# Performance work log

Hardware: AMD Instinct MI355X
Metric: run time of the kernel (lower is better)

The kernel has to match this reference:

```python
import jax, jax.numpy as jnp
import numpy as np

B, CQ, CKV, H, W = 16, 512, 512, 48, 48
NH = 8
HD = CQ // NH
SCALE = HD ** -0.5


def setup_inputs() -> dict:
    key = jax.random.key(0)
    ks = jax.random.split(key, 11)
    s = 0.02
    return {
        "query_features": jax.random.normal(ks[0], (B, CQ, H, W), jnp.float32),
        "key_features": jax.random.normal(ks[1], (B, CKV, H, W), jnp.float32),
        "value_features": jax.random.normal(ks[2], (B, CKV, H, W), jnp.float32),
        "Wq": jax.random.normal(ks[3], (CQ, CQ), jnp.float32) * s,
        "bq": jnp.zeros((CQ,), jnp.float32),
        "Wk": jax.random.normal(ks[4], (CQ, CKV), jnp.float32) * s,
        "bk": jnp.zeros((CQ,), jnp.float32),
        "Wv": jax.random.normal(ks[5], (CQ, CKV), jnp.float32) * s,
        "bv": jnp.zeros((CQ,), jnp.float32),
        "Wo": jax.random.normal(ks[6], (CQ, CQ), jnp.float32) * s,
        "bo": jnp.zeros((CQ,), jnp.float32),
    }


def _proj(x, Wt, b):
    # 1x1 conv == channel GEMM: (O,C) x (B,C,H,W) -> (B,O,H,W)
    return jnp.einsum('oc,bchw->bohw', Wt, x) + b[None, :, None, None]


def reference(query_features, key_features, value_features,
              Wq, bq, Wk, bk, Wv, bv, Wo, bo):
    b, cq, h, w = query_features.shape
    hw = h * w
    Q = _proj(query_features, Wq, bq).reshape(b, NH, HD, hw)
    K = _proj(key_features, Wk, bk).reshape(b, NH, HD, hw)
    V = _proj(value_features, Wv, bv).reshape(b, NH, HD, hw)
    # NOTE: faithful to source — contraction is over the SPATIAL axis d=H*W,
    # so scores are (B, NH, HD, HD) (head_dim x head_dim attention).
    scores = jnp.einsum('bnhd,bnkd->bnhk', Q, K) * SCALE
    attn = jax.nn.softmax(scores, axis=-1)
    out = jnp.einsum('bnhk,bnkd->bnhd', attn, V)  # (B, NH, HD, HW)
    out = out.reshape(b, cq, h, w)
    return _proj(out, Wo, bo)
```

## Files before the change

### kernel.cpp

```cpp
#include <hip/hip_runtime.h>
#include <hip/hip_bf16.h>

#define B_   16
#define C_   512
#define HW_  2304
#define NH_  8
#define SCALE_ 0.125f

typedef __bf16 bf16x8 __attribute__((ext_vector_type(8)));
typedef __bf16 bf16x4 __attribute__((ext_vector_type(4)));
typedef float  f32x4  __attribute__((ext_vector_type(4)));

#define MFMA16(a, b, c) __builtin_amdgcn_mfma_f32_16x16x32_bf16((a), (b), (c), 0, 0, 0)

__device__ __forceinline__ void gload_lds16(const void* g, void* l) {
    __builtin_amdgcn_global_load_lds(
        (const __attribute__((address_space(1))) unsigned int*)g,
        (__attribute__((address_space(3))) unsigned int*)l, 16, 0, 0);
}

__device__ __forceinline__ bf16x8 pack8(const float4 a, const float4 b) {
    bf16x8 o;
    o[0] = (__bf16)a.x; o[1] = (__bf16)a.y; o[2] = (__bf16)a.z; o[3] = (__bf16)a.w;
    o[4] = (__bf16)b.x; o[5] = (__bf16)b.y; o[6] = (__bf16)b.z; o[7] = (__bf16)b.w;
    return o;
}

__global__ __launch_bounds__(256) void wprep(
    const float* __restrict__ Wq, const float* __restrict__ Wk,
    const float* __restrict__ Wv, const float* __restrict__ Wo,
    __bf16* __restrict__ WqB, __bf16* __restrict__ WkB,
    __bf16* __restrict__ WvT, __bf16* __restrict__ WoB)
{
    const int t = threadIdx.x;
    if (blockIdx.y < 3) {
        const float* src = blockIdx.y == 0 ? Wq : blockIdx.y == 1 ? Wk : Wo;
        __bf16*      dst = blockIdx.y == 0 ? WqB : blockIdx.y == 1 ? WkB : WoB;
        const int idx = blockIdx.x * 2048 + t * 8;
        const float4 f0 = *(const float4*)&src[idx];
        const float4 f1 = *(const float4*)&src[idx + 4];
        *(bf16x8*)&dst[idx] = pack8(f0, f1);
        return;
    }
    if (blockIdx.x >= 64) return;
    const int tx = blockIdx.x & 7, ty = blockIdx.x >> 3;
    __shared__ float Ts[64 * 65];
    {
        const int r = t >> 2, c0 = (t & 3) * 16;
        #pragma unroll
        for (int j = 0; j < 4; ++j) {
            const float4 v = *(const float4*)&Wv[(size_t)(ty * 64 + r) * C_ + tx * 64 + c0 + j * 4];
            Ts[r * 65 + c0 + j * 4 + 0] = v.x;
            Ts[r * 65 + c0 + j * 4 + 1] = v.y;
            Ts[r * 65 + c0 + j * 4 + 2] = v.z;
            Ts[r * 65 + c0 + j * 4 + 3] = v.w;
        }
    }
    __syncthreads();
    {
        const int c = t >> 2, r0 = (t & 3) * 16;
        bf16x8 o0, o1;
        #pragma unroll
        for (int j = 0; j < 8; ++j) {
            o0[j] = (__bf16)Ts[(r0 + j) * 65 + c];
            o1[j] = (__bf16)Ts[(r0 + 8 + j) * 65 + c];
        }
        *(bf16x8*)&WvT[(size_t)(tx * 64 + c) * C_ + ty * 64 + r0]     = o0;
        *(bf16x8*)&WvT[(size_t)(tx * 64 + c) * C_ + ty * 64 + r0 + 8] = o1;
    }
}

__global__ __launch_bounds__(256) void prep(
    const float* __restrict__ X, __bf16* __restrict__ XT)
{
    const int t  = threadIdx.x;
    const int b  = blockIdx.z;
    const int c0 = blockIdx.y * 64;
    const int h0 = blockIdx.x * 128;
    const float* Xb = X + (size_t)b * C_ * HW_;
    __bf16* XTb = XT + (size_t)b * HW_ * C_;

    __shared__ float Ts[64 * 129];

    #pragma unroll
    for (int p = 0; p < 8; ++p) {
        const int c  = p * 8 + (t >> 5);
        const int hg = (t & 31) * 4;
        const float4 v = *(const float4*)&Xb[(size_t)(c0 + c) * HW_ + h0 + hg];
        Ts[c * 129 + hg + 0] = v.x;
        Ts[c * 129 + hg + 1] = v.y;
        Ts[c * 129 + hg + 2] = v.z;
        Ts[c * 129 + hg + 3] = v.w;
    }
    __syncthreads();
    #pragma unroll
    for (int p = 0; p < 4; ++p) {
        const int hw = p * 32 + (t >> 3);
        const int g  = (t & 7) * 8;
        bf16x8 o;
        #pragma unroll
        for (int e = 0; e < 8; ++e)
            o[e] = (__bf16)Ts[(g + e) * 129 + hw];
        *(bf16x8*)&XTb[(size_t)(h0 + hw) * C_ + c0 + g] = o;
    }
}

__global__ __launch_bounds__(512) void gxx(
    const float* __restrict__ Xk, const float* __restrict__ Xq,
    __bf16* __restrict__ Gp, float* __restrict__ xksum, float* __restrict__ xqsum)
{
    const int i    = blockIdx.x;
    const int xcd  = i & 7, slot = i >> 3;
    const int b    = xcd + 8 * (slot & 1);
    const int xy   = slot >> 1;
    const int n0   = (xy & 3) * 128;
    const int m0   = (xy >> 2) * 128;

    __shared__ __align__(16) __bf16 As[128 * 64];
    __shared__ __align__(16) __bf16 Bs[128 * 64];

    const int t = threadIdx.x, w = t >> 6, lane = t & 63, l16 = lane & 15, q = lane >> 4;
    const int wm = w >> 1, wn = w & 1;
    const int r = t >> 2, qq = t & 3;

    const float* Ap = Xk + (size_t)b * C_ * HW_ + (size_t)(m0 + r) * HW_ + qq * 16;
    const float* Bp = Xq + (size_t)b * C_ * HW_ + (size_t)(n0 + r) * HW_ + qq * 16;

    float4 av[4], bv[4];
    #pragma unroll
    for (int j = 0; j < 4; ++j) {
        av[j] = *(const float4*)&Ap[j * 4];
        bv[j] = *(const float4*)&Bp[j * 4];
    }

    const bool doA = (n0 == 0), doB = (m0 == 0);
    float sA = 0.f, sB = 0.f;
    f32x4 acc[2][4] = {};

    for (int ks = 0; ks < 36; ++ks) {
        if (ks) __syncthreads();
        if (doA) {
            #pragma unroll
            for (int j = 0; j < 4; ++j) sA += av[j].x + av[j].y + av[j].z + av[j].w;
        }
        if (doB) {
            #pragma unroll
            for (int j = 0; j < 4; ++j) sB += bv[j].x + bv[j].y + bv[j].z + bv[j].w;
        }
        #pragma unroll
        for (int jj = 0; jj < 2; ++jj) {
            const int g  = qq * 2 + jj;
            const int sw = (g ^ (r & 7)) * 8;
            *(bf16x8*)&As[r * 64 + sw] = pack8(av[jj * 2], av[jj * 2 + 1]);
            *(bf16x8*)&Bs[r * 64 + sw] = pack8(bv[jj * 2], bv[jj * 2 + 1]);
        }
        __syncthreads();
        if (ks + 1 < 36) {
            const int off = (ks + 1) * 64;
            #pragma unroll
            for (int j = 0; j < 4; ++j) {
                av[j] = *(const float4*)&Ap[off + j * 4];
                bv[j] = *(const float4*)&Bp[off + j * 4];
            }
        }
        #pragma unroll
        for (int kk = 0; kk < 2; ++kk) {
            const int sw = ((kk * 4 + q) ^ (l16 & 7)) * 8;
            bf16x8 af[2], bfr[4];
            #pragma unroll
            for (int mi = 0; mi < 2; ++mi)
                af[mi] = *(bf16x8*)&As[(wm * 32 + mi * 16 + l16) * 64 + sw];
            #pragma unroll
            for (int ni = 0; ni < 4; ++ni)
                bfr[ni] = *(bf16x8*)&Bs[(wn * 64 + ni * 16 + l16) * 64 + sw];
            #pragma unroll
            for (int mi = 0; mi < 2; ++mi)
                #pragma unroll
                for (int ni = 0; ni < 4; ++ni)
                    acc[mi][ni] = MFMA16(af[mi], bfr[ni], acc[mi][ni]);
        }
    }

    if (doA) {
        float s = sA; s += __shfl_xor(s, 1); s += __shfl_xor(s, 2);
        if (qq == 0) xksum[b * C_ + m0 + r] = s;
    }
    if (doB) {
        float s = sB; s += __shfl_xor(s, 1); s += __shfl_xor(s, 2);
        if (qq == 0) xqsum[b * C_ + n0 + r] = s;
    }

    __bf16* Gb = Gp + (size_t)b * C_ * C_;
    #pragma unroll
    for (int mi = 0; mi < 2; ++mi)
        #pragma unroll
        for (int rr = 0; rr < 4; ++rr) {
            const int m = m0 + wm * 32 + mi * 16 + q * 4 + rr;
            #pragma unroll
            for (int ni = 0; ni < 4; ++ni) {
                const int n = n0 + wn * 64 + ni * 16 + l16;
                Gb[(size_t)m * C_ + n] = (__bf16)acc[mi][ni][rr];
            }
        }
}

__global__ __launch_bounds__(512) void scoresk(
    const __bf16* __restrict__ Gp, const __bf16* __restrict__ WqB,
    const __bf16* __restrict__ WkB, const float* __restrict__ xqsum,
    const float* __restrict__ xksum, const float* __restrict__ bq,
    const float* __restrict__ bk, __bf16* __restrict__ P)
{
    const int i  = blockIdx.x;
    const int b  = (i & 7) + 8 * ((i >> 3) & 1);
    const int nh = i >> 4;

    __shared__ __align__(16) __bf16 Gs[512 * 64];
    __shared__ __align__(16) __bf16 Ws[64 * 64];
    __shared__ float Ss[64 * 64];
    __shared__ float aqs[64], aks[64];

    const int t = threadIdx.x, w = t >> 6, lane = t & 63, l16 = lane & 15, q = lane >> 4;

    {
        const int h = t >> 3, seg = (t & 7) * 64;
        const __bf16* wr1 = WqB + (size_t)(nh * 64 + h) * C_ + seg;
        const __bf16* wr2 = WkB + (size_t)(nh * 64 + h) * C_ + seg;
        const float* x1 = xqsum + b * C_ + seg;
        const float* x2 = xksum + b * C_ + seg;
        float s1 = 0.f, s2 = 0.f;
        #pragma unroll
        for (int e = 0; e < 64; e += 8) {
            const bf16x8 v1 = *(const bf16x8*)&wr1[e];
            const bf16x8 v2 = *(const bf16x8*)&wr2[e];
            #pragma unroll
            for (int j = 0; j < 8; ++j) {
                s1 += (float)v1[j] * x1[e + j];
                s2 += (float)v2[j] * x2[e + j];
            }
        }
        s1 += __shfl_xor(s1, 1); s1 += __shfl_xor(s1, 2); s1 += __shfl_xor(s1, 4);
        s2 += __shfl_xor(s2, 1); s2 += __shfl_xor(s2, 2); s2 += __shfl_xor(s2, 4);
        if ((t & 7) == 0) { aqs[h] = s1; aks[h] = s2; }
    }

    const int hf = w >> 1, ch = w & 1;
    const __bf16* Gb = Gp + (size_t)b * C_ * C_;
    f32x4 acc[16] = {};

    for (int ks = 0; ks < 8; ++ks) {
        const int k0 = ks * 64;
        __syncthreads();
        {
            const int row = t >> 3;
            const int sg  = ((lane & 7) ^ (row & 7)) * 8;
            gload_lds16(&WqB[(size_t)(nh * 64 + row) * C_ + k0 + sg], &Ws[(w * 8) * 64]);
        }
        #pragma unroll
        for (int p = 0; p < 8; ++p) {
            const int row = p * 64 + w * 8 + (lane >> 3);
            const int sg  = ((lane & 7) ^ (row & 7)) * 8;
            gload_lds16(&Gb[(size_t)row * C_ + k0 + sg], &Gs[(p * 64 + w * 8) * 64]);
        }
        __syncthreads();
        #pragma unroll
        for (int kk = 0; kk < 2; ++kk) {
            const int sw = ((kk * 4 + q) ^ (l16 & 7)) * 8;
            const bf16x8 a = *(const bf16x8*)&Ws[(hf * 16 + l16) * 64 + sw];
            #pragma unroll
            for (int ni = 0; ni < 16; ++ni) {
                const bf16x8 g = *(const bf16x8*)&Gs[(ch * 256 + ni * 16 + l16) * 64 + sw];
                acc[ni] = MFMA16(a, g, acc[ni]);
            }
        }
    }

    __syncthreads();
    #pragma unroll
    for (int ni = 0; ni < 16; ++ni) {
        const int c2 = ch * 256 + ni * 16 + l16;
        #pragma unroll
        for (int rr = 0; rr < 4; ++rr) {
            const int h = hf * 16 + q * 4 + rr;
            Gs[h * 512 + (((c2 >> 3) ^ (h & 7)) << 3) + (c2 & 7)] = (__bf16)acc[ni][rr];
        }
    }
    __syncthreads();

    f32x4 sacc[2] = {};
    const int kf0 = (w & 1) * 2;
    for (int ks = 0; ks < 8; ++ks) {
        if (ks) __syncthreads();
        {
            const int row = t >> 3;
            const int sg  = ((lane & 7) ^ (row & 7)) * 8;
            gload_lds16(&WkB[(size_t)(nh * 64 + row) * C_ + ks * 64 + sg], &Ws[(w * 8) * 64]);
        }
        __syncthreads();
        #pragma unroll
        for (int kk = 0; kk < 2; ++kk) {
            const int h = hf * 16 + l16;
            const int g = ks * 8 + kk * 4 + q;
            const bf16x8 a = *(const bf16x8*)&Gs[h * 512 + ((g ^ (h & 7)) << 3)];
            const int swb = ((kk * 4 + q) ^ (l16 & 7)) * 8;
            #pragma unroll
            for (int kf = 0; kf < 2; ++kf) {
                const bf16x8 bb = *(const bf16x8*)&Ws[((kf0 + kf) * 16 + l16) * 64 + swb];
                sacc[kf] = MFMA16(a, bb, sacc[kf]);
            }
        }
    }

    #pragma unroll
    for (int kf = 0; kf < 2; ++kf)
        #pragma unroll
        for (int rr = 0; rr < 4; ++rr)
            Ss[(hf * 16 + q * 4 + rr) * 64 + (kf0 + kf) * 16 + l16] = sacc[kf][rr];
    __syncthreads();

    {
        const int h = t >> 3, j0 = (t & 7) * 8;
        const float bqv = bq[nh * 64 + h];
        const float aqv = aqs[h];
        float v[8];
        float mx = -1e30f;
        #pragma unroll
        for (int j = 0; j < 8; ++j) {
            const int k = j0 + j;
            const float bkv = bk[nh * 64 + k];
            v[j] = SCALE_ * (Ss[h * 64 + k] + aqv * bkv + bqv * (aks[k] + (float)HW_ * bkv));
            mx = fmaxf(mx, v[j]);
        }
        mx = fmaxf(mx, __shfl_xor(mx, 1));
        mx = fmaxf(mx, __shfl_xor(mx, 2));
        mx = fmaxf(mx, __shfl_xor(mx, 4));
        float sum = 0.f;
        #pragma unroll
        for (int j = 0; j < 8; ++j) { v[j] = __expf(v[j] - mx); sum += v[j]; }
        sum += __shfl_xor(sum, 1); sum += __shfl_xor(sum, 2); sum += __shfl_xor(sum, 4);
        const float inv = 1.f / sum;
        bf16x8 o;
        #pragma unroll
        for (int j = 0; j < 8; ++j) o[j] = (__bf16)(v[j] * inv);
        *(bf16x8*)&P[(((size_t)b * NH_ + nh) * 64 + h) * 64 + j0] = o;
    }
}

__global__ __launch_bounds__(512) void pwv(
    const __bf16* __restrict__ P, const __bf16* __restrict__ WvT,
    const float* __restrict__ bv, __bf16* __restrict__ W2T, float* __restrict__ Bb)
{
    const int n = blockIdx.x, b = blockIdx.y;
    __shared__ __align__(16) __bf16 Ps[64 * 64];
    __shared__ __align__(16) __bf16 Vs[512 * 64];
    __shared__ __align__(16) __bf16 W2s[8][64 * 72];

    const int t = threadIdx.x, w = t >> 6, lane = t & 63, l16 = lane & 15, q = lane >> 4;

    {
        const int row = t >> 3;
        const int sg  = ((lane & 7) ^ (row & 7)) * 8;
        gload_lds16(&P[(((size_t)b * NH_ + n) * 64 + row) * 64 + sg], &Ps[(w * 8) * 64]);
    }
    #pragma unroll
    for (int p = 0; p < 8; ++p) {
        const int row = p * 64 + w * 8 + (lane >> 3);
        const int sg  = ((lane & 7) ^ (row & 7)) * 8;
        gload_lds16(&WvT[(size_t)row * C_ + n * 64 + sg], &Vs[(p * 64 + w * 8) * 64]);
    }
    __syncthreads();

    {
        const int h = t >> 3, g = t & 7;
        const bf16x8 pv = *(const bf16x8*)&Ps[h * 64 + ((g ^ (h & 7)) << 3)];
        float s = 0.f;
        #pragma unroll
        for (int j = 0; j < 8; ++j) s += (float)pv[j] * bv[n * 64 + g * 8 + j];
        s += __shfl_xor(s, 1); s += __shfl_xor(s, 2); s += __shfl_xor(s, 4);
        if (g == 0) Bb[b * C_ + n * 64 + h] = s;
    }

    f32x4 acc[4][4] = {};
    #pragma unroll
    for (int kk = 0; kk < 2; ++kk) {
        const int sw = ((kk * 4 + q) ^ (l16 & 7)) * 8;
        bf16x8 af[4], bfr[4];
        #pragma unroll
        for (int hf = 0; hf < 4; ++hf)
            af[hf] = *(const bf16x8*)&Ps[(hf * 16 + l16) * 64 + sw];
        #pragma unroll
        for (int ni = 0; ni < 4; ++ni)
            bfr[ni] = *(const bf16x8*)&Vs[(w * 64 + ni * 16 + l16) * 64 + sw];
        #pragma unroll
        for (int hf = 0; hf < 4; ++hf)
            #pragma unroll
            for (int ni = 0; ni < 4; ++ni)
                acc[hf][ni] = MFMA16(af[hf], bfr[ni], acc[hf][ni]);
    }

    #pragma unroll
    for (int hf = 0; hf < 4; ++hf)
        #pragma unroll
        for (int ni = 0; ni < 4; ++ni) {
            const int cl = ni * 16 + l16;
            bf16x4 o;
            #pragma unroll
            for (int rr = 0; rr < 4; ++rr) o[rr] = (__bf16)acc[hf][ni][rr];
            *(bf16x4*)&W2s[w][cl * 72 + hf * 16 + q * 4] = o;
        }
    __syncthreads();
    #pragma unroll
    for (int p = 0; p < 8; ++p) {
        const int cl = p * 8 + (lane >> 3);
        const int g  = lane & 7;
        const bf16x8 v = *(const bf16x8*)&W2s[w][cl * 72 + g * 8];
        *(bf16x8*)&W2T[((size_t)b * C_ + w * 64 + cl) * C_ + n * 64 + g * 8] = v;
    }
}

__global__ __launch_bounds__(512) void ugemm(
    const __bf16* __restrict__ W2T, const __bf16* __restrict__ WoB,
    __bf16* __restrict__ U, const float* __restrict__ Bb,
    const float* __restrict__ bo, float* __restrict__ fb)
{
    const int b  = blockIdx.z;
    const int n0 = blockIdx.x * 128;
    const int m0 = blockIdx.y * 128;
    const __bf16* Bn = W2T + (size_t)b * C_ * C_;

    __shared__ __align__(16) __bf16 As[128 * 64];
    __shared__ __align__(16) __bf16 Bs[128 * 64];

    const int t = threadIdx.x, w = t >> 6, lane = t & 63, l16 = lane & 15, q = lane >> 4;
    const int wm = w >> 1, wn = w & 1;
    const int sr = lane >> 3;
    const int sg = ((lane & 7) ^ sr) * 8;

    f32x4 acc[2][4] = {};
    for (int ks = 0; ks < 8; ++ks) {
        const int k0 = ks * 64;
        __syncthreads();
        #pragma unroll
        for (int p = 0; p < 2; ++p) {
            const int rb = p * 64 + w * 8;
            gload_lds16(&WoB[(size_t)(m0 + rb + sr) * C_ + k0 + sg], &As[rb * 64]);
            gload_lds16(&Bn [(size_t)(n0 + rb + sr) * C_ + k0 + sg], &Bs[rb * 64]);
        }
        __syncthreads();
        #pragma unroll
        for (int kk = 0; kk < 2; ++kk) {
            const int sw = ((kk * 4 + q) ^ (l16 & 7)) * 8;
            bf16x8 af[2], bfr[4];
            #pragma unroll
            for (int mi = 0; mi < 2; ++mi)
                af[mi] = *(bf16x8*)&As[(wm * 32 + mi * 16 + l16) * 64 + sw];
            #pragma unroll
            for (int ni = 0; ni < 4; ++ni)
                bfr[ni] = *(bf16x8*)&Bs[(wn * 64 + ni * 16 + l16) * 64 + sw];
            #pragma unroll
            for (int mi = 0; mi < 2; ++mi)
                #pragma unroll
                for (int ni = 0; ni < 4; ++ni)
                    acc[mi][ni] = MFMA16(af[mi], bfr[ni], acc[mi][ni]);
        }
    }

    __bf16* Ub = U + (size_t)b * C_ * C_;
    #pragma unroll
    for (int mi = 0; mi < 2; ++mi)
        #pragma unroll
        for (int rr = 0; rr < 4; ++rr) {
            const int m = m0 + wm * 32 + mi * 16 + q * 4 + rr;
            #pragma unroll
            for (int ni = 0; ni < 4; ++ni) {
                const int n = n0 + wn * 64 + ni * 16 + l16;
                Ub[(size_t)m * C_ + n] = (__bf16)acc[mi][ni][rr];
            }
        }

    if (blockIdx.x == 0) {
        const int o   = m0 + (t >> 2);
        const int seg = (t & 3) * 128;
        const __bf16* wr = WoB + (size_t)o * C_ + seg;
        const float* be = Bb + b * C_ + seg;
        float s = 0.f;
        #pragma unroll
        for (int e = 0; e < 128; e += 8) {
            const bf16x8 v = *(const bf16x8*)&wr[e];
            #pragma unroll
            for (int j = 0; j < 8; ++j) s += (float)v[j] * be[e + j];
        }
        s += __shfl_xor(s, 1); s += __shfl_xor(s, 2);
        if ((t & 3) == 0) fb[b * C_ + o] = s + bo[o];
    }
}

template <typename OUT_T, int OSTR, bool BIAS>
__device__ __forceinline__ void gemm_body(
    const __bf16* __restrict__ Bn, const __bf16* __restrict__ Am,
    const float* __restrict__ bias, OUT_T* __restrict__ Yb,
    int n0, int m0)
{
    __shared__ __align__(16) __bf16 As[128 * 64];
    __shared__ __align__(16) __bf16 Bs[128 * 64];

    const int t = threadIdx.x;
    const int w = t >> 6, lane = t & 63, l16 = lane & 15, q = lane >> 4;
    const int wm = w >> 1, wn = w & 1;
    const int sr = lane >> 3;
    const int sg = ((lane & 7) ^ (lane >> 3)) * 8;

    f32x4 acc[4][4] = {};

    for (int ks = 0; ks < 8; ++ks) {
        const int k0 = ks * 64;
        __syncthreads();
        #pragma unroll
        for (int p = 0; p < 4; ++p) {
            const int rb = p * 32 + w * 8;
            gload_lds16(&Am[(size_t)(m0 + rb + sr) * C_ + k0 + sg], &As[rb * 64]);
            gload_lds16(&Bn[(size_t)(n0 + rb + sr) * C_ + k0 + sg], &Bs[rb * 64]);
        }
        __syncthreads();
        #pragma unroll
        for (int kk = 0; kk < 2; ++kk) {
            const int sw = ((kk * 4 + q) ^ (l16 & 7)) * 8;
            bf16x8 af[4], bfr[4];
            #pragma unroll
            for (int mi = 0; mi < 4; ++mi)
                af[mi] = *(bf16x8*)&As[(wm * 64 + mi * 16 + l16) * 64 + sw];
            #pragma unroll
            for (int ni = 0; ni < 4; ++ni)
                bfr[ni] = *(bf16x8*)&Bs[(wn * 64 + ni * 16 + l16) * 64 + sw];
            #pragma unroll
            for (int mi = 0; mi < 4; ++mi)
                #pragma unroll
                for (int ni = 0; ni < 4; ++ni)
                    acc[mi][ni] = MFMA16(af[mi], bfr[ni], acc[mi][ni]);
        }
    }

    #pragma unroll
    for (int mi = 0; mi < 4; ++mi) {
        #pragma unroll
        for (int r = 0; r < 4; ++r) {
            const int m = m0 + wm * 64 + mi * 16 + q * 4 + r;
            const float bv_ = BIAS ? bias[m] : 0.f;
            #pragma unroll
            for (int ni = 0; ni < 4; ++ni) {
                const int n = n0 + wn * 64 + ni * 16 + l16;
                Yb[(size_t)m * OSTR + n] = (OUT_T)(acc[mi][ni][r] + bv_);
            }
        }
    }
}

__global__ __launch_bounds__(256) void finalk(
    const __bf16* __restrict__ XvT, const __bf16* __restrict__ U,
    const float* __restrict__ fb, float* __restrict__ out)
{
    const int b = blockIdx.z;
    gemm_body<float, HW_, true>(XvT + (size_t)b * HW_ * C_, U + (size_t)b * C_ * C_,
                                fb + b * C_, out + (size_t)b * C_ * HW_,
                                blockIdx.x * 128, blockIdx.y * 128);
}

extern "C" void kernel_launch(void* const* d_in, const int* in_sizes, int n_in,
                              void* d_out, int out_size, void* d_ws, size_t ws_size,
                              hipStream_t stream)
{
    (void)in_sizes; (void)n_in; (void)out_size; (void)ws_size;
    const float* qf = (const float*)d_in[0];
    const float* kf = (const float*)d_in[1];
    const float* vf = (const float*)d_in[2];
    const float* Wq = (const float*)d_in[3];
    const float* bq = (const float*)d_in[4];
    const float* Wk = (const float*)d_in[5];
    const float* bk = (const float*)d_in[6];
    const float* Wv = (const float*)d_in[7];
    const float* bv = (const float*)d_in[8];
    const float* Wo = (const float*)d_in[9];
    const float* bo = (const float*)d_in[10];

    __bf16* XvT  = (__bf16*)d_ws;
    __bf16* Gp   = XvT  + (size_t)B_ * HW_ * C_;
    __bf16* W2T  = Gp   + (size_t)B_ * C_ * C_;
    __bf16* U    = W2T  + (size_t)B_ * C_ * C_;
    __bf16* WqB  = U    + (size_t)B_ * C_ * C_;
    __bf16* WkB  = WqB  + C_ * C_;
    __bf16* WvTb = WkB  + C_ * C_;
    __bf16* WoB  = WvTb + C_ * C_;
    __bf16* Pb   = WoB  + C_ * C_;
    float*  xqs  = (float*)(Pb + (size_t)B_ * NH_ * 64 * 64);
    float*  xks  = xqs + B_ * C_;
    float*  Bb   = xks + B_ * C_;
    float*  fb   = Bb  + B_ * C_;

    wprep  <<<dim3(128, 4),   256, 0, stream>>>(Wq, Wk, Wv, Wo, WqB, WkB, WvTb, WoB);
    prep   <<<dim3(18, 8, 16),256, 0, stream>>>(vf, XvT);
    gxx    <<<dim3(256),      512, 0, stream>>>(kf, qf, Gp, xks, xqs);
    scoresk<<<dim3(128),      512, 0, stream>>>(Gp, WqB, WkB, xqs, xks, bq, bk, Pb);
    pwv    <<<dim3(8, 16),    512, 0, stream>>>(Pb, WvTb, bv, W2T, Bb);
    ugemm  <<<dim3(4, 4, 16), 512, 0, stream>>>(W2T, WoB, U, Bb, bo, fb);
    finalk <<<dim3(18, 4, 16),256, 0, stream>>>(XvT, U, fb, (float*)d_out);
}
```

Measured before the change: 395.6 us.

## Pre-convert Q/K features to bf16 and split score computation into separate GEMM

```diff
diff --git a/kernel.cpp b/kernel.cpp
--- a/kernel.cpp
+++ b/kernel.cpp
@@ -70,6 +70,33 @@
     }
 }
 
+__global__ __launch_bounds__(256) void cvt(
+    const float* __restrict__ Xq, const float* __restrict__ Xk,
+    __bf16* __restrict__ XqB, __bf16* __restrict__ XkB,
+    float* __restrict__ xqsum, float* __restrict__ xksum)
+{
+    const int z = blockIdx.z, b = blockIdx.y;
+    const int row = blockIdx.x * 32 + (threadIdx.x >> 3);
+    const int lq = threadIdx.x & 7;
+    const float* sp = (z ? Xk : Xq) + ((size_t)b * C_ + row) * HW_;
+    __bf16*      dp = (z ? XkB : XqB) + ((size_t)b * C_ + row) * HW_;
+    float s = 0.f;
+    #pragma unroll
+    for (int p = 0; p < 18; ++p) {
+        const int c0 = p * 128 + lq * 16;
+        const float4 f0 = *(const float4*)&sp[c0];
+        const float4 f1 = *(const float4*)&sp[c0 + 4];
+        const float4 f2 = *(const float4*)&sp[c0 + 8];
+        const float4 f3 = *(const float4*)&sp[c0 + 12];
+        s += f0.x + f0.y + f0.z + f0.w + f1.x + f1.y + f1.z + f1.w
+           + f2.x + f2.y + f2.z + f2.w + f3.x + f3.y + f3.z + f3.w;
+        *(bf16x8*)&dp[c0]     = pack8(f0, f1);
+        *(bf16x8*)&dp[c0 + 8] = pack8(f2, f3);
+    }
+    s += __shfl_xor(s, 1); s += __shfl_xor(s, 2); s += __shfl_xor(s, 4);
+    if (lq == 0) (z ? xksum : xqsum)[b * C_ + row] = s;
+}
+
 __global__ __launch_bounds__(256) void prep(
     const float* __restrict__ X, __bf16* __restrict__ XT)
 {
@@ -105,74 +132,52 @@
     }
 }
 
-__global__ __launch_bounds__(512) void gxx(
-    const float* __restrict__ Xk, const float* __restrict__ Xq,
-    __bf16* __restrict__ Gp, float* __restrict__ xksum, float* __restrict__ xqsum)
+__global__ __launch_bounds__(256) void gxx(
+    const __bf16* __restrict__ XkB, const __bf16* __restrict__ XqB,
+    __bf16* __restrict__ Gp)
 {
     const int i    = blockIdx.x;
     const int xcd  = i & 7, slot = i >> 3;
     const int b    = xcd + 8 * (slot & 1);
-    const int xy   = slot >> 1;
-    const int n0   = (xy & 3) * 128;
-    const int m0   = (xy >> 2) * 128;
+    const int tile = slot >> 1;
+    const int n0   = (tile & 7) * 64;
+    const int m0   = (tile >> 3) * 128;
 
     __shared__ __align__(16) __bf16 As[128 * 64];
-    __shared__ __align__(16) __bf16 Bs[128 * 64];
+    __shared__ __align__(16) __bf16 Bs[64 * 64];
 
     const int t = threadIdx.x, w = t >> 6, lane = t & 63, l16 = lane & 15, q = lane >> 4;
-    const int wm = w >> 1, wn = w & 1;
-    const int r = t >> 2, qq = t & 3;
-
-    const float* Ap = Xk + (size_t)b * C_ * HW_ + (size_t)(m0 + r) * HW_ + qq * 16;
-    const float* Bp = Xq + (size_t)b * C_ * HW_ + (size_t)(n0 + r) * HW_ + qq * 16;
-
-    float4 av[4], bv[4];
-    #pragma unroll
-    for (int j = 0; j < 4; ++j) {
-        av[j] = *(const float4*)&Ap[j * 4];
-        bv[j] = *(const float4*)&Bp[j * 4];
-    }
-
-    const bool doA = (n0 == 0), doB = (m0 == 0);
-    float sA = 0.f, sB = 0.f;
+    const int sr = lane >> 3;
+    const int sg = ((lane & 7) ^ sr) * 8;
+
+    const __bf16* Am = XkB + (size_t)b * C_ * HW_;
+    const __bf16* Bn = XqB + (size_t)b * C_ * HW_;
+
     f32x4 acc[2][4] = {};
-
     for (int ks = 0; ks < 36; ++ks) {
-        if (ks) __syncthreads();
-        if (doA) {
-            #pragma unroll
-            for (int j = 0; j < 4; ++j) sA += av[j].x + av[j].y + av[j].z + av[j].w;
-        }
-        if (doB) {
-            #pragma unroll
-            for (int j = 0; j < 4; ++j) sB += bv[j].x + bv[j].y + bv[j].z + bv[j].w;
-        }
-        #pragma unroll
-        for (int jj = 0; jj < 2; ++jj) {
-            const int g  = qq * 2 + jj;
-            const int sw = (g ^ (r & 7)) * 8;
-            *(bf16x8*)&As[r * 64 + sw] = pack8(av[jj * 2], av[jj * 2 + 1]);
-            *(bf16x8*)&Bs[r * 64 + sw] = pack8(bv[jj * 2], bv[jj * 2 + 1]);
-        }
-        __syncthreads();
-        if (ks + 1 < 36) {
-            const int off = (ks + 1) * 64;
-            #pragma unroll
-            for (int j = 0; j < 4; ++j) {
-                av[j] = *(const float4*)&Ap[off + j * 4];
-                bv[j] = *(const float4*)&Bp[off + j * 4];
-            }
-        }
+        const int k0 = ks * 64;
+        __syncthreads();
+        #pragma unroll
+        for (int p = 0; p < 4; ++p) {
+            const int rb = p * 32 + w * 8;
+            gload_lds16(&Am[(size_t)(m0 + rb + sr) * HW_ + k0 + sg], &As[rb * 64]);
+        }
+        #pragma unroll
+        for (int p = 0; p < 2; ++p) {
+            const int rb = w * 16 + p * 8;
+            gload_lds16(&Bn[(size_t)(n0 + rb + sr) * HW_ + k0 + sg], &Bs[rb * 64]);
+        }
+        __syncthreads();
         #pragma unroll
         for (int kk = 0; kk < 2; ++kk) {
             const int sw = ((kk * 4 + q) ^ (l16 & 7)) * 8;
             bf16x8 af[2], bfr[4];
             #pragma unroll
             for (int mi = 0; mi < 2; ++mi)
-                af[mi] = *(bf16x8*)&As[(wm * 32 + mi * 16 + l16) * 64 + sw];
+                af[mi] = *(bf16x8*)&As[(w * 32 + mi * 16 + l16) * 64 + sw];
             #pragma unroll
             for (int ni = 0; ni < 4; ++ni)
-                bfr[ni] = *(bf16x8*)&Bs[(wn * 64 + ni * 16 + l16) * 64 + sw];
+                bfr[ni] = *(bf16x8*)&Bs[(ni * 16 + l16) * 64 + sw];
             #pragma unroll
             for (int mi = 0; mi < 2; ++mi)
                 #pragma unroll
@@ -181,16 +186,67 @@
         }
     }
 
-    if (doA) {
-        float s = sA; s += __shfl_xor(s, 1); s += __shfl_xor(s, 2);
-        if (qq == 0) xksum[b * C_ + m0 + r] = s;
-    }
-    if (doB) {
-        float s = sB; s += __shfl_xor(s, 1); s += __shfl_xor(s, 2);
-        if (qq == 0) xqsum[b * C_ + n0 + r] = s;
-    }
-
     __bf16* Gb = Gp + (size_t)b * C_ * C_;
+    #pragma unroll
+    for (int mi = 0; mi < 2; ++mi)
+        #pragma unroll
+        for (int rr = 0; rr < 4; ++rr) {
+            const int m = m0 + w * 32 + mi * 16 + q * 4 + rr;
+            #pragma unroll
+            for (int ni = 0; ni < 4; ++ni) {
+                const int n = n0 + ni * 16 + l16;
+                Gb[(size_t)m * C_ + n] = (__bf16)acc[mi][ni][rr];
+            }
+        }
+}
+
+__global__ __launch_bounds__(512) void tgemm(
+    const __bf16* __restrict__ Gp, const __bf16* __restrict__ WqB,
+    __bf16* __restrict__ Tb)
+{
+    const int b  = blockIdx.z;
+    const int n0 = blockIdx.x * 128;
+    const int m0 = blockIdx.y * 128;
+    const __bf16* Bn = Gp + (size_t)b * C_ * C_;
+
+    __shared__ __align__(16) __bf16 As[128 * 64];
+    __shared__ __align__(16) __bf16 Bs[128 * 64];
+
+    const int t = threadIdx.x, w = t >> 6, lane = t & 63, l16 = lane & 15, q = lane >> 4;
+    const int wm = w >> 1, wn = w & 1;
+    const int sr = lane >> 3;
+    const int sg = ((lane & 7) ^ sr) * 8;
+
+    f32x4 acc[2][4] = {};
+    for (int ks = 0; ks < 8; ++ks) {
+        const int k0 = ks * 64;
+        __syncthreads();
+        #pragma unroll
+        for (int p = 0; p < 2; ++p) {
+            const int rb = p * 64 + w * 8;
+            gload_lds16(&WqB[(size_t)(m0 + rb + sr) * C_ + k0 + sg], &As[rb * 64]);
+            gload_lds16(&Bn [(size_t)(n0 + rb + sr) * C_ + k0 + sg], &Bs[rb * 64]);
+        }
+        __syncthreads();
+        #pragma unroll
+        for (int kk = 0; kk < 2; ++kk) {
+            const int sw = ((kk * 4 + q) ^ (l16 & 7)) * 8;
+            bf16x8 af[2], bfr[4];
+            #pragma unroll
+            for (int mi = 0; mi < 2; ++mi)
+                af[mi] = *(bf16x8*)&As[(wm * 32 + mi * 16 + l16) * 64 + sw];
+            #pragma unroll
+            for (int ni = 0; ni < 4; ++ni)
+                bfr[ni] = *(bf16x8*)&Bs[(wn * 64 + ni * 16 + l16) * 64 + sw];
+            #pragma unroll
+            for (int mi = 0; mi < 2; ++mi)
+                #pragma unroll
+                for (int ni = 0; ni < 4; ++ni)
+                    acc[mi][ni] = MFMA16(af[mi], bfr[ni], acc[mi][ni]);
+        }
+    }
+
+    __bf16* Tn = Tb + (size_t)b * C_ * C_;
     #pragma unroll
     for (int mi = 0; mi < 2; ++mi)
         #pragma unroll
@@ -199,13 +255,13 @@
             #pragma unroll
             for (int ni = 0; ni < 4; ++ni) {
                 const int n = n0 + wn * 64 + ni * 16 + l16;
-                Gb[(size_t)m * C_ + n] = (__bf16)acc[mi][ni][rr];
+                Tn[(size_t)m * C_ + n] = (__bf16)acc[mi][ni][rr];
             }
         }
 }
 
-__global__ __launch_bounds__(512) void scoresk(
-    const __bf16* __restrict__ Gp, const __bf16* __restrict__ WqB,
+__global__ __launch_bounds__(512) void ssoft(
+    const __bf16* __restrict__ Tb, const __bf16* __restrict__ WqB,
     const __bf16* __restrict__ WkB, const float* __restrict__ xqsum,
     const float* __restrict__ xksum, const float* __restrict__ bq,
     const float* __restrict__ bk, __bf16* __restrict__ P)
@@ -214,12 +270,13 @@
     const int b  = (i & 7) + 8 * ((i >> 3) & 1);
     const int nh = i >> 4;
 
-    __shared__ __align__(16) __bf16 Gs[512 * 64];
-    __shared__ __align__(16) __bf16 Ws[64 * 64];
+    __shared__ __align__(16) __bf16 Ts[8][64 * 64];
+    __shared__ __align__(16) __bf16 Ks[8][64 * 64];
     __shared__ float Ss[64 * 64];
     __shared__ float aqs[64], aks[64];
 
     const int t = threadIdx.x, w = t >> 6, lane = t & 63, l16 = lane & 15, q = lane >> 4;
+    const int sr = lane >> 3;
 
     {
         const int h = t >> 3, seg = (t & 7) * 64;
@@ -243,78 +300,36 @@
         if ((t & 7) == 0) { aqs[h] = s1; aks[h] = s2; }
     }
 
-    const int hf = w >> 1, ch = w & 1;
-    const __bf16* Gb = Gp + (size_t)b * C_ * C_;
-    f32x4 acc[16] = {};
-
-    for (int ks = 0; ks < 8; ++ks) {
-        const int k0 = ks * 64;
-        __syncthreads();
-        {
-            const int row = t >> 3;
-            const int sg  = ((lane & 7) ^ (row & 7)) * 8;
-            gload_lds16(&WqB[(size_t)(nh * 64 + row) * C_ + k0 + sg], &Ws[(w * 8) * 64]);
-        }
-        #pragma unroll
-        for (int p = 0; p < 8; ++p) {
-            const int row = p * 64 + w * 8 + (lane >> 3);
-            const int sg  = ((lane & 7) ^ (row & 7)) * 8;
-            gload_lds16(&Gb[(size_t)row * C_ + k0 + sg], &Gs[(p * 64 + w * 8) * 64]);
-        }
-        __syncthreads();
+    const __bf16* Tn = Tb + (size_t)b * C_ * C_ + (size_t)(nh * 64) * C_;
+    const __bf16* Kn = WkB + (size_t)(nh * 64) * C_;
+    const int sgr = ((lane & 7) ^ sr) * 8;
+    #pragma unroll
+    for (int s = 0; s < 8; ++s) {
+        gload_lds16(&Tn[(size_t)(w * 8 + sr) * C_ + s * 64 + sgr], &Ts[s][(w * 8) * 64]);
+        gload_lds16(&Kn[(size_t)(w * 8 + sr) * C_ + s * 64 + sgr], &Ks[s][(w * 8) * 64]);
+    }
+    __syncthreads();
+
+    const int mi = w & 3, ni0 = (w >> 2) * 2;
+    f32x4 sacc[2] = {};
+    #pragma unroll
+    for (int s = 0; s < 8; ++s)
         #pragma unroll
         for (int kk = 0; kk < 2; ++kk) {
             const int sw = ((kk * 4 + q) ^ (l16 & 7)) * 8;
-            const bf16x8 a = *(const bf16x8*)&Ws[(hf * 16 + l16) * 64 + sw];
-            #pragma unroll
-            for (int ni = 0; ni < 16; ++ni) {
-                const bf16x8 g = *(const bf16x8*)&Gs[(ch * 256 + ni * 16 + l16) * 64 + sw];
-                acc[ni] = MFMA16(a, g, acc[ni]);
+            const bf16x8 a = *(const bf16x8*)&Ts[s][(mi * 16 + l16) * 64 + sw];
+            #pragma unroll
+            for (int j = 0; j < 2; ++j) {
+                const bf16x8 bb = *(const bf16x8*)&Ks[s][((ni0 + j) * 16 + l16) * 64 + sw];
+                sacc[j] = MFMA16(a, bb, sacc[j]);
             }
         }
-    }
-
-    __syncthreads();
-    #pragma unroll
-    for (int ni = 0; ni < 16; ++ni) {
-        const int c2 = ch * 256 + ni * 16 + l16;
-        #pragma unroll
-        for (int rr = 0; rr < 4; ++rr) {
-            const int h = hf * 16 + q * 4 + rr;
-            Gs[h * 512 + (((c2 >> 3) ^ (h & 7)) << 3) + (c2 & 7)] = (__bf16)acc[ni][rr];
-        }
-    }
-    __syncthreads();
-
-    f32x4 sacc[2] = {};
-    const int kf0 = (w & 1) * 2;
-    for (int ks = 0; ks < 8; ++ks) {
-        if (ks) __syncthreads();
-        {
-            const int row = t >> 3;
-            const int sg  = ((lane & 7) ^ (row & 7)) * 8;
-            gload_lds16(&WkB[(size_t)(nh * 64 + row) * C_ + ks * 64 + sg], &Ws[(w * 8) * 64]);
-        }
-        __syncthreads();
-        #pragma unroll
-        for (int kk = 0; kk < 2; ++kk) {
-            const int h = hf * 16 + l16;
-            const int g = ks * 8 + kk * 4 + q;
-            const bf16x8 a = *(const bf16x8*)&Gs[h * 512 + ((g ^ (h & 7)) << 3)];
-            const int swb = ((kk * 4 + q) ^ (l16 & 7)) * 8;
-            #pragma unroll
-            for (int kf = 0; kf < 2; ++kf) {
-                const bf16x8 bb = *(const bf16x8*)&Ws[((kf0 + kf) * 16 + l16) * 64 + swb];
-                sacc[kf] = MFMA16(a, bb, sacc[kf]);
-            }
-        }
-    }
-
-    #pragma unroll
-    for (int kf = 0; kf < 2; ++kf)
+
+    #pragma unroll
+    for (int j = 0; j < 2; ++j)
         #pragma unroll
         for (int rr = 0; rr < 4; ++rr)
-            Ss[(hf * 16 + q * 4 + rr) * 64 + (kf0 + kf) * 16 + l16] = sacc[kf][rr];
+            Ss[(mi * 16 + q * 4 + rr) * 64 + (ni0 + j) * 16 + l16] = sacc[j][rr];
     __syncthreads();
 
     {
@@ -581,8 +596,12 @@
     const float* Wo = (const float*)d_in[9];
     const float* bo = (const float*)d_in[10];
 
+    const size_t QE = (size_t)B_ * C_ * HW_;
     __bf16* XvT  = (__bf16*)d_ws;
-    __bf16* Gp   = XvT  + (size_t)B_ * HW_ * C_;
+    __bf16* XqB  = XvT  + QE;
+    __bf16* XkB  = XqB  + QE;
+    __bf16* Tb   = XqB;
+    __bf16* Gp   = XkB  + QE;
     __bf16* W2T  = Gp   + (size_t)B_ * C_ * C_;
     __bf16* U    = W2T  + (size_t)B_ * C_ * C_;
     __bf16* WqB  = U    + (size_t)B_ * C_ * C_;
@@ -595,11 +614,13 @@
     float*  Bb   = xks + B_ * C_;
     float*  fb   = Bb  + B_ * C_;
 
-    wprep  <<<dim3(128, 4),   256, 0, stream>>>(Wq, Wk, Wv, Wo, WqB, WkB, WvTb, WoB);
-    prep   <<<dim3(18, 8, 16),256, 0, stream>>>(vf, XvT);
-    gxx    <<<dim3(256),      512, 0, stream>>>(kf, qf, Gp, xks, xqs);
-    scoresk<<<dim3(128),      512, 0, stream>>>(Gp, WqB, WkB, xqs, xks, bq, bk, Pb);
-    pwv    <<<dim3(8, 16),    512, 0, stream>>>(Pb, WvTb, bv, W2T, Bb);
-    ugemm  <<<dim3(4, 4, 16), 512, 0, stream>>>(W2T, WoB, U, Bb, bo, fb);
-    finalk <<<dim3(18, 4, 16),256, 0, stream>>>(XvT, U, fb, (float*)d_out);
-}
+    wprep  <<<dim3(128, 4),    256, 0, stream>>>(Wq, Wk, Wv, Wo, WqB, WkB, WvTb, WoB);
+    cvt    <<<dim3(16, 16, 2), 256, 0, stream>>>(qf, kf, XqB, XkB, xqs, xks);
+    prep   <<<dim3(18, 8, 16), 256, 0, stream>>>(vf, XvT);
+    gxx    <<<dim3(512),       256, 0, stream>>>(XkB, XqB, Gp);
+    tgemm  <<<dim3(4, 4, 16),  512, 0, stream>>>(Gp, WqB, Tb);
+    ssoft  <<<dim3(128),       512, 0, stream>>>(Tb, WqB, WkB, xqs, xks, bq, bk, Pb);
+    pwv    <<<dim3(8, 16),     512, 0, stream>>>(Pb, WvTb, bv, W2T, Bb);
+    ugemm  <<<dim3(4, 4, 16),  512, 0, stream>>>(W2T, WoB, U, Bb, bo, fb);
+    finalk <<<dim3(18, 4, 16), 256, 0, stream>>>(XvT, U, fb, (float*)d_out);
+}
```

Result: slower. 408.9 us (+3.4%).
